# Optimization experiments

Hardware: AMD Instinct MI355X
Metric: run time of the kernel (lower is better)

The kernel has to match this reference:

```python
import jax, jax.numpy as jnp
import numpy as np

N = 50000      # nodes
E = 800000     # edges
IN = 128       # in_channels
HID = 128      # hidden_channels
R = 8          # num_relations
B = 4          # num_bases
EPS = 1e-5     # BatchNorm eps


def setup_inputs() -> dict:
    key = jax.random.key(0)
    ks = jax.random.split(key, 16)
    s = 0.05
    f = jnp.float32
    return {
        "x": jax.random.normal(ks[0], (N, IN), f),
        "edge_index": jax.random.randint(ks[1], (2, E), 0, N),
        "edge_type": jax.random.randint(ks[2], (E,), 0, R),
        # conv1 (RGCNConv with basis decomposition): W_r = sum_b comp[r,b] * bases[b]
        "comp1": jax.random.normal(ks[3], (R, B), f) * s,
        "bases1": jax.random.normal(ks[4], (B, IN, HID), f) * s,
        "root1": jax.random.normal(ks[5], (IN, HID), f) * s,
        "bias1": jnp.zeros((HID,), f),
        # skip1: Linear(in, hidden)
        "skip1_w": jax.random.normal(ks[6], (IN, HID), f) * s,
        "skip1_b": jnp.zeros((HID,), f),
        # BatchNorm(hidden)
        "bn_gamma": jnp.ones((HID,), f),
        "bn_beta": jnp.zeros((HID,), f),
        # conv2
        "comp2": jax.random.normal(ks[7], (R, B), f) * s,
        "bases2": jax.random.normal(ks[8], (B, HID, HID), f) * s,
        "root2": jax.random.normal(ks[9], (HID, HID), f) * s,
        "bias2": jnp.zeros((HID,), f),
        # skip2: Linear(hidden, hidden)
        "skip2_w": jax.random.normal(ks[10], (HID, HID), f) * s,
        "skip2_b": jnp.zeros((HID,), f),
    }


def rgcn_conv(x, src, dst, etype, comp, bases, root, bias):
    """PyG RGCNConv: per-relation mean aggregation + root weight + bias."""
    # Basis decomposition: W [R, d_in, d_out]
    W = jnp.einsum('rb,bdf->rdf', comp, bases)
    # Transform all nodes under every relation (node-level GEMM, avoids [E,B,F])
    h = jnp.einsum('nd,rdf->rnf', x, W)          # [R, N, F]
    msg = h[etype, src]                           # [E, F] gather per edge
    # mean per (dst, relation): normalize by relation-specific in-degree
    seg = dst * R + etype                         # combined segment id
    cnt = jax.ops.segment_sum(jnp.ones((msg.shape[0],), x.dtype), seg,
                              num_segments=N * R)
    msg = msg * (1.0 / jnp.maximum(cnt, 1.0))[seg][:, None]
    agg = jax.ops.segment_sum(msg, dst, num_segments=N)  # sum over relations
    return agg + x @ root + bias


def reference(x, edge_index, edge_type,
              comp1, bases1, root1, bias1, skip1_w, skip1_b,
              bn_gamma, bn_beta,
              comp2, bases2, root2, bias2, skip2_w, skip2_b):
    src, dst = edge_index[0], edge_index[1]
    # layer 1: conv + skip
    x1 = rgcn_conv(x, src, dst, edge_type, comp1, bases1, root1, bias1) \
         + x @ skip1_w + skip1_b
    h = x1  # captured pre-BatchNorm (i == num_layers - 1 branch)
    # BatchNorm (training-style batch stats) + ReLU; dropout = identity (eval)
    m = x1.mean(axis=0)
    v = x1.var(axis=0)
    xn = bn_gamma * (x1 - m) / jnp.sqrt(v + EPS) + bn_beta
    xr = jax.nn.relu(xn)
    # final layer: conv + skip
    x2 = rgcn_conv(xr, src, dst, edge_type, comp2, bases2, root2, bias2) \
         + xr @ skip2_w + skip2_b
    return (h, x2)
```

## Files before the change

kernel.cpp:

```cpp
#include <hip/hip_runtime.h>
#include <hip/hip_bf16.h>

#define Nn   50000
#define Ee   800000
#define RR   8
#define CAP  64
#define EPSV 1e-5f
#define NBLK 1563
#define NSLICE 8
#define SLICE_N 6250

typedef unsigned int   u32;
typedef unsigned short u16;
typedef __attribute__((ext_vector_type(8))) short bf16x8;
typedef __attribute__((ext_vector_type(4))) float f32x4;

typedef __attribute__((address_space(1))) const void gvoid;
typedef __attribute__((address_space(3))) void lvoid;

__device__ __forceinline__ void gl_lds16(const void* g, void* l) {
    __builtin_amdgcn_global_load_lds((gvoid*)g, (lvoid*)l, 16, 0, 0);
}

__device__ __forceinline__ float bf2f(u16 u) {
    return __uint_as_float(((u32)u) << 16);
}
__device__ __forceinline__ u16 f2bf(float f) {
    u32 x = __float_as_uint(f);
    u32 r = (x + 0x7FFFu + ((x >> 16) & 1u)) >> 16;
    return (u16)r;
}
__device__ __forceinline__ u32 pack2(float a, float b) {
    return (u32)f2bf(a) | ((u32)f2bf(b) << 16);
}

__global__ void __launch_bounds__(256) setup(
        const float2* __restrict__ xf, u32* __restrict__ xb,
        const int* __restrict__ ei, const int* __restrict__ et,
        int* __restrict__ deg, int* __restrict__ buckets,
        const float* __restrict__ bases1, const float* __restrict__ root1,
        const float* __restrict__ skip1w, u16* __restrict__ wt1,
        const float* __restrict__ bases2, const float* __restrict__ root2,
        const float* __restrict__ skip2w, u16* __restrict__ wt2) {
    int b = blockIdx.x;
    if (b < 12500) {
        int t = b * 256 + threadIdx.x;
        float2 v = xf[t];
        xb[t] = pack2(v.x, v.y);
    } else if (b < 37500) {
        int bb = b - 12500;
        int slice = bb & 7;
        int e = (bb >> 3) * 256 + threadIdx.x;
        int dst = ei[Ee + e];
        if ((u32)(dst - slice * SLICE_N) < (u32)SLICE_N) {
            int src = ei[e];
            int rt  = et[e];
            int idx = atomicAdd(&deg[dst], 1);
            if (idx < CAP)
                buckets[dst * CAP + idx] = (src & 0xFFFF) | (rt << 16);
        }
    } else {
        const float *bs, *ro, *sk; u16* wt; int t;
        if (b < 37820) { t = (b - 37500) * 256 + threadIdx.x; bs = bases1; ro = root1; sk = skip1w; wt = wt1; }
        else           { t = (b - 37820) * 256 + threadIdx.x; bs = bases2; ro = root2; sk = skip2w; wt = wt2; }
        int c = t / 640, k = t % 640;
        float v;
        if (k < 512) {
            int bb = k >> 7, kk = k & 127;
            v = bs[(bb * 128 + kk) * 128 + c];
        } else {
            int kk = k - 512;
            v = ro[kk * 128 + c] + sk[kk * 128 + c];
        }
        wt[c * 640 + k] = f2bf(v);
    }
}

__global__ void __launch_bounds__(256, 8) aggregate(const u32* __restrict__ xrow,
                                                    const float* __restrict__ comp,
                                                    const int* __restrict__ deg,
                                                    const int* __restrict__ buckets,
                                                    u32* __restrict__ xcat) {
    __shared__ int   bk_s[4][CAP];
    __shared__ float scale_s[4][32];
    int wv = threadIdx.x >> 6, lane = threadIdx.x & 63;
    int node = blockIdx.x * 4 + wv;

    int d = deg[node];
    d = d < CAP ? d : CAP;
    const int* bk = buckets + node * CAP;

    int w0 = 0;
    if (lane < d) { w0 = bk[lane]; bk_s[wv][lane] = w0; }

    int rt0 = (lane < d) ? (w0 >> 16) : 8;
    int c[RR];
#pragma unroll
    for (int r = 0; r < RR; r++) c[r] = __popcll(__ballot(rt0 == r));

    if (lane < 32) {
        int cc = c[lane >> 2];
        scale_s[wv][lane] = comp[lane] / (float)(cc < 1 ? 1 : cc);
    }
    __syncthreads();

    float a0 = 0, a1 = 0, b0 = 0, b1 = 0, c0 = 0, c1 = 0, d0 = 0, d1 = 0;
    int i = 0;
    for (; i + 4 <= d; i += 4) {
        int e0 = bk_s[wv][i], e1 = bk_s[wv][i + 1];
        int e2 = bk_s[wv][i + 2], e3 = bk_s[wv][i + 3];
        u32 x0 = xrow[(e0 & 0xFFFF) * 64 + lane];
        u32 x1 = xrow[(e1 & 0xFFFF) * 64 + lane];
        u32 x2 = xrow[(e2 & 0xFFFF) * 64 + lane];
        u32 x3 = xrow[(e3 & 0xFFFF) * 64 + lane];
        f32x4 s0 = *(const f32x4*)&scale_s[wv][(e0 >> 16) * 4];
        f32x4 s1 = *(const f32x4*)&scale_s[wv][(e1 >> 16) * 4];
        f32x4 s2 = *(const f32x4*)&scale_s[wv][(e2 >> 16) * 4];
        f32x4 s3 = *(const f32x4*)&scale_s[wv][(e3 >> 16) * 4];
        float v0, v1;
        v0 = bf2f((u16)x0); v1 = bf2f((u16)(x0 >> 16));
        a0 += s0[0] * v0; a1 += s0[0] * v1; b0 += s0[1] * v0; b1 += s0[1] * v1;
        c0 += s0[2] * v0; c1 += s0[2] * v1; d0 += s0[3] * v0; d1 += s0[3] * v1;
        v0 = bf2f((u16)x1); v1 = bf2f((u16)(x1 >> 16));
        a0 += s1[0] * v0; a1 += s1[0] * v1; b0 += s1[1] * v0; b1 += s1[1] * v1;
        c0 += s1[2] * v0; c1 += s1[2] * v1; d0 += s1[3] * v0; d1 += s1[3] * v1;
        v0 = bf2f((u16)x2); v1 = bf2f((u16)(x2 >> 16));
        a0 += s2[0] * v0; a1 += s2[0] * v1; b0 += s2[1] * v0; b1 += s2[1] * v1;
        c0 += s2[2] * v0; c1 += s2[2] * v1; d0 += s2[3] * v0; d1 += s2[3] * v1;
        v0 = bf2f((u16)x3); v1 = bf2f((u16)(x3 >> 16));
        a0 += s3[0] * v0; a1 += s3[0] * v1; b0 += s3[1] * v0; b1 += s3[1] * v1;
        c0 += s3[2] * v0; c1 += s3[2] * v1; d0 += s3[3] * v0; d1 += s3[3] * v1;
    }
    for (; i < d; i++) {
        int ee = bk_s[wv][i];
        u32 xv = xrow[(ee & 0xFFFF) * 64 + lane];
        f32x4 ss = *(const f32x4*)&scale_s[wv][(ee >> 16) * 4];
        float v0 = bf2f((u16)xv), v1 = bf2f((u16)(xv >> 16));
        a0 += ss[0] * v0; a1 += ss[0] * v1; b0 += ss[1] * v0; b1 += ss[1] * v1;
        c0 += ss[2] * v0; c1 += ss[2] * v1; d0 += ss[3] * v0; d1 += ss[3] * v1;
    }

    u32* orow = xcat + node * 256;
    orow[0 * 64 + lane] = pack2(a0, a1);
    orow[1 * 64 + lane] = pack2(b0, b1);
    orow[2 * 64 + lane] = pack2(c0, c1);
    orow[3 * 64 + lane] = pack2(d0, d1);
}

__global__ void __launch_bounds__(256) gemm_x(const u16* __restrict__ xcat,
                                              const u16* __restrict__ xrow,
                                              const u16* __restrict__ wt,
                                              const float* __restrict__ biasA,
                                              const float* __restrict__ biasB,
                                              float* __restrict__ out,
                                              float* __restrict__ bnsum,
                                              int do_stats) {
    __shared__ u16 As[32 * 64];
    __shared__ u16 Bs[128 * 64];

    int t = threadIdx.x, w = t >> 6, lane = t & 63;
    int m0 = blockIdx.x * 32;
    int lm = lane & 15, hk = lane >> 4;

    const u16* agp; const u16* axp; char* alp;
    {
        int f = t;
        int row = f >> 3, kc = (f & 7) ^ (row & 7);
        int gr = m0 + row; gr = gr < Nn ? gr : Nn - 1;
        agp = xcat + gr * 512 + kc * 8;
        axp = xrow + gr * 128 + kc * 8;
        alp = (char*)As + w * 1024;
    }
    const u16* bgp[4]; char* blp[4];
#pragma unroll
    for (int j = 0; j < 4; j++) {
        int f = j * 256 + t;
        int col = f >> 3, kc = (f & 7) ^ (col & 7);
        bgp[j] = wt + col * 640 + kc * 8;
        blp[j] = (char*)Bs + j * 4096 + w * 1024;
    }

    int wr = (w & 1) * 16, wc = (w >> 1) * 64;
    f32x4 acc[4];
#pragma unroll
    for (int g = 0; g < 4; g++) acc[g] = (f32x4){0, 0, 0, 0};

    for (int it = 0; it < 10; it++) {
        if (it < 8) gl_lds16(agp + it * 64, alp);
        else        gl_lds16(axp + (it - 8) * 64, alp);
        int kb = it * 64;
#pragma unroll
        for (int j = 0; j < 4; j++) gl_lds16(bgp[j] + kb, blp[j]);
        __syncthreads();
#pragma unroll
        for (int ks = 0; ks < 2; ks++) {
            int sw = (((ks * 4 + hk) ^ (lm & 7)) * 16);
            bf16x8 a0 = *(const bf16x8*)((const char*)As + (wr + lm) * 128 + sw);
            bf16x8 b0 = *(const bf16x8*)((const char*)Bs + (wc + lm) * 128 + sw);
            bf16x8 b1 = *(const bf16x8*)((const char*)Bs + (wc + 16 + lm) * 128 + sw);
            bf16x8 b2 = *(const bf16x8*)((const char*)Bs + (wc + 32 + lm) * 128 + sw);
            bf16x8 b3 = *(const bf16x8*)((const char*)Bs + (wc + 48 + lm) * 128 + sw);
            acc[0] = __builtin_amdgcn_mfma_f32_16x16x32_bf16(a0, b0, acc[0], 0, 0, 0);
            acc[1] = __builtin_amdgcn_mfma_f32_16x16x32_bf16(a0, b1, acc[1], 0, 0, 0);
            acc[2] = __builtin_amdgcn_mfma_f32_16x16x32_bf16(a0, b2, acc[2], 0, 0, 0);
            acc[3] = __builtin_amdgcn_mfma_f32_16x16x32_bf16(a0, b3, acc[3], 0, 0, 0);
        }
        __syncthreads();
    }

    float bias[4];
#pragma unroll
    for (int g = 0; g < 4; g++) {
        int cc = wc + g * 16 + lm;
        bias[g] = biasA[cc] + biasB[cc];
    }
    float lsum[4] = {0, 0, 0, 0}, lsq[4] = {0, 0, 0, 0};
#pragma unroll
    for (int g = 0; g < 4; g++)
#pragma unroll
        for (int i = 0; i < 4; i++) {
            int grow = m0 + wr + hk * 4 + i;
            if (grow < Nn) {
                float v = acc[g][i] + bias[g];
                out[grow * 128 + wc + g * 16 + lm] = v;
                lsum[g] += v; lsq[g] += v * v;
            }
        }
    if (do_stats) {
#pragma unroll
        for (int g = 0; g < 4; g++) {
            lsum[g] += __shfl_xor(lsum[g], 16); lsum[g] += __shfl_xor(lsum[g], 32);
            lsq[g]  += __shfl_xor(lsq[g], 16);  lsq[g]  += __shfl_xor(lsq[g], 32);
        }
        if (hk == 0) {
#pragma unroll
            for (int g = 0; g < 4; g++) {
                int cc = wc + g * 16 + lm;
                atomicAdd(&bnsum[cc], lsum[g]);
                atomicAdd(&bnsum[128 + cc], lsq[g]);
            }
        }
    }
}

__global__ void __launch_bounds__(256) bn_relu(const float2* __restrict__ h,
                                               const float* __restrict__ bnsum,
                                               const float* __restrict__ gamma,
                                               const float* __restrict__ beta,
                                               u32* __restrict__ xr) {
    __shared__ float ab_s[256];
    int tid = threadIdx.x;
    if (tid < 128) {
        float m   = bnsum[tid] * (1.0f / Nn);
        float ex2 = bnsum[128 + tid] * (1.0f / Nn);
        float var = ex2 - m * m;
        float s   = gamma[tid] * rsqrtf(var + EPSV);
        ab_s[tid]       = s;
        ab_s[128 + tid] = beta[tid] - m * s;
    }
    __syncthreads();
    int t = blockIdx.x * 256 + tid;
    int c0 = (tid & 63) * 2;
    float2 hv = h[t];
    float v0 = hv.x * ab_s[c0] + ab_s[128 + c0];
    float v1 = hv.y * ab_s[c0 + 1] + ab_s[128 + c0 + 1];
    v0 = v0 > 0.f ? v0 : 0.f;
    v1 = v1 > 0.f ? v1 : 0.f;
    xr[t] = pack2(v0, v1);
}

extern "C" void kernel_launch(void* const* d_in, const int* in_sizes, int n_in,
                              void* d_out, int out_size, void* d_ws, size_t ws_size,
                              hipStream_t stream) {
    const float* x      = (const float*)d_in[0];
    const int*   ei     = (const int*)d_in[1];
    const int*   et     = (const int*)d_in[2];
    const float* comp1  = (const float*)d_in[3];
    const float* bases1 = (const float*)d_in[4];
    const float* root1  = (const float*)d_in[5];
    const float* bias1  = (const float*)d_in[6];
    const float* skip1w = (const float*)d_in[7];
    const float* skip1b = (const float*)d_in[8];
    const float* gamma  = (const float*)d_in[9];
    const float* beta   = (const float*)d_in[10];
    const float* comp2  = (const float*)d_in[11];
    const float* bases2 = (const float*)d_in[12];
    const float* root2  = (const float*)d_in[13];
    const float* bias2  = (const float*)d_in[14];
    const float* skip2w = (const float*)d_in[15];
    const float* skip2b = (const float*)d_in[16];
    float* out = (float*)d_out;

    char* ws = (char*)d_ws;
    int*   deg     = (int*)(ws + 0);
    float* bnsum   = (float*)(ws + 200000);
    int*   buckets = (int*)(ws + 202240);
    u16*   wt1     = (u16*)(ws + 13002240);
    u16*   wt2     = (u16*)(ws + 13166080);
    u32*   xb      = (u32*)(ws + 13329920);
    u32*   xr      = xb;
    u16*   xcat    = (u16*)(ws + 26129920);

    hipMemsetAsync(deg, 0, 201024, stream);

    setup<<<38140, 256, 0, stream>>>((const float2*)x, xb, ei, et, deg, buckets,
                                     bases1, root1, skip1w, wt1,
                                     bases2, root2, skip2w, wt2);

    aggregate<<<Nn / 4, 256, 0, stream>>>(xb, comp1, deg, buckets, (u32*)xcat);
    gemm_x<<<NBLK, 256, 0, stream>>>(xcat, (const u16*)xb, wt1, bias1, skip1b,
                                     out, bnsum, 1);

    bn_relu<<<Nn / 4, 256, 0, stream>>>((const float2*)out, bnsum, gamma, beta, xr);

    aggregate<<<Nn / 4, 256, 0, stream>>>(xr, comp2, deg, buckets, (u32*)xcat);
    gemm_x<<<NBLK, 256, 0, stream>>>(xcat, (const u16*)xr, wt2, bias2, skip2b,
                                     out + Nn * 128, bnsum, 0);
}
```

Baseline: 344.8 us.

## Rewrite gemm_x as LDS-free per-wave 32x128 tiles with direct global loads

New measurement: 364.0 us. 5.6% more time.

```diff
diff --git a/kernel.cpp b/kernel.cpp
--- a/kernel.cpp
+++ b/kernel.cpp
@@ -6,7 +6,7 @@
 #define RR   8
 #define CAP  64
 #define EPSV 1e-5f
-#define NBLK 1563
+#define NBLK 391
 #define NSLICE 8
 #define SLICE_N 6250
 
@@ -17,10 +17,6 @@
 
 typedef __attribute__((address_space(1))) const void gvoid;
 typedef __attribute__((address_space(3))) void lvoid;
-
-__device__ __forceinline__ void gl_lds16(const void* g, void* l) {
-    __builtin_amdgcn_global_load_lds((gvoid*)g, (lvoid*)l, 16, 0, 0);
-}
 
 __device__ __forceinline__ float bf2f(u16 u) {
     return __uint_as_float(((u32)u) << 16);
@@ -147,95 +143,84 @@
     orow[3 * 64 + lane] = pack2(d0, d1);
 }
 
-__global__ void __launch_bounds__(256) gemm_x(const u16* __restrict__ xcat,
-                                              const u16* __restrict__ xrow,
-                                              const u16* __restrict__ wt,
-                                              const float* __restrict__ biasA,
-                                              const float* __restrict__ biasB,
-                                              float* __restrict__ out,
-                                              float* __restrict__ bnsum,
-                                              int do_stats) {
-    __shared__ u16 As[32 * 64];
-    __shared__ u16 Bs[128 * 64];
-
+__global__ void __launch_bounds__(256, 1) gemm_x(const u16* __restrict__ xcat,
+                                                 const u16* __restrict__ xrow,
+                                                 const u16* __restrict__ wt,
+                                                 const float* __restrict__ biasA,
+                                                 const float* __restrict__ biasB,
+                                                 float* __restrict__ out,
+                                                 float* __restrict__ bnsum,
+                                                 int do_stats) {
     int t = threadIdx.x, w = t >> 6, lane = t & 63;
-    int m0 = blockIdx.x * 32;
     int lm = lane & 15, hk = lane >> 4;
-
-    const u16* agp; const u16* axp; char* alp;
-    {
-        int f = t;
-        int row = f >> 3, kc = (f & 7) ^ (row & 7);
-        int gr = m0 + row; gr = gr < Nn ? gr : Nn - 1;
-        agp = xcat + gr * 512 + kc * 8;
-        axp = xrow + gr * 128 + kc * 8;
-        alp = (char*)As + w * 1024;
-    }
-    const u16* bgp[4]; char* blp[4];
-#pragma unroll
-    for (int j = 0; j < 4; j++) {
-        int f = j * 256 + t;
-        int col = f >> 3, kc = (f & 7) ^ (col & 7);
-        bgp[j] = wt + col * 640 + kc * 8;
-        blp[j] = (char*)Bs + j * 4096 + w * 1024;
-    }
-
-    int wr = (w & 1) * 16, wc = (w >> 1) * 64;
-    f32x4 acc[4];
-#pragma unroll
-    for (int g = 0; g < 4; g++) acc[g] = (f32x4){0, 0, 0, 0};
-
+    int mw = (blockIdx.x * 4 + w) * 32;
+
+    int r0 = mw + lm;      r0 = r0 < Nn ? r0 : Nn - 1;
+    int r1 = mw + 16 + lm; r1 = r1 < Nn ? r1 : Nn - 1;
+    const u16* a0p = xcat + r0 * 512 + hk * 8;
+    const u16* a1p = xcat + r1 * 512 + hk * 8;
+    const u16* x0p = xrow + r0 * 128 + hk * 8;
+    const u16* x1p = xrow + r1 * 128 + hk * 8;
+    const u16* bp  = wt + lm * 640 + hk * 8;
+
+    f32x4 acc[2][8];
+#pragma unroll
+    for (int fr = 0; fr < 2; fr++)
+#pragma unroll
+        for (int g = 0; g < 8; g++) acc[fr][g] = (f32x4){0, 0, 0, 0};
+
+#pragma unroll
     for (int it = 0; it < 10; it++) {
-        if (it < 8) gl_lds16(agp + it * 64, alp);
-        else        gl_lds16(axp + (it - 8) * 64, alp);
-        int kb = it * 64;
-#pragma unroll
-        for (int j = 0; j < 4; j++) gl_lds16(bgp[j] + kb, blp[j]);
-        __syncthreads();
 #pragma unroll
         for (int ks = 0; ks < 2; ks++) {
-            int sw = (((ks * 4 + hk) ^ (lm & 7)) * 16);
-            bf16x8 a0 = *(const bf16x8*)((const char*)As + (wr + lm) * 128 + sw);
-            bf16x8 b0 = *(const bf16x8*)((const char*)Bs + (wc + lm) * 128 + sw);
-            bf16x8 b1 = *(const bf16x8*)((const char*)Bs + (wc + 16 + lm) * 128 + sw);
-            bf16x8 b2 = *(const bf16x8*)((const char*)Bs + (wc + 32 + lm) * 128 + sw);
-            bf16x8 b3 = *(const bf16x8*)((const char*)Bs + (wc + 48 + lm) * 128 + sw);
-            acc[0] = __builtin_amdgcn_mfma_f32_16x16x32_bf16(a0, b0, acc[0], 0, 0, 0);
-            acc[1] = __builtin_amdgcn_mfma_f32_16x16x32_bf16(a0, b1, acc[1], 0, 0, 0);
-            acc[2] = __builtin_amdgcn_mfma_f32_16x16x32_bf16(a0, b2, acc[2], 0, 0, 0);
-            acc[3] = __builtin_amdgcn_mfma_f32_16x16x32_bf16(a0, b3, acc[3], 0, 0, 0);
-        }
-        __syncthreads();
-    }
-
-    float bias[4];
-#pragma unroll
-    for (int g = 0; g < 4; g++) {
-        int cc = wc + g * 16 + lm;
-        bias[g] = biasA[cc] + biasB[cc];
-    }
-    float lsum[4] = {0, 0, 0, 0}, lsq[4] = {0, 0, 0, 0};
-#pragma unroll
-    for (int g = 0; g < 4; g++)
-#pragma unroll
-        for (int i = 0; i < 4; i++) {
-            int grow = m0 + wr + hk * 4 + i;
-            if (grow < Nn) {
-                float v = acc[g][i] + bias[g];
-                out[grow * 128 + wc + g * 16 + lm] = v;
-                lsum[g] += v; lsq[g] += v * v;
+            int ko = it * 64 + ks * 32;
+            bf16x8 a0, a1;
+            if (it < 8) {
+                a0 = *(const bf16x8*)(a0p + ko);
+                a1 = *(const bf16x8*)(a1p + ko);
+            } else {
+                int kx = (it - 8) * 64 + ks * 32;
+                a0 = *(const bf16x8*)(x0p + kx);
+                a1 = *(const bf16x8*)(x1p + kx);
             }
+#pragma unroll
+            for (int g = 0; g < 8; g++) {
+                bf16x8 b = *(const bf16x8*)(bp + g * 10240 + ko);
+                acc[0][g] = __builtin_amdgcn_mfma_f32_16x16x32_bf16(a0, b, acc[0][g], 0, 0, 0);
+                acc[1][g] = __builtin_amdgcn_mfma_f32_16x16x32_bf16(a1, b, acc[1][g], 0, 0, 0);
+            }
+        }
+    }
+
+    float lsum[8], lsq[8];
+#pragma unroll
+    for (int g = 0; g < 8; g++) { lsum[g] = 0.f; lsq[g] = 0.f; }
+#pragma unroll
+    for (int fr = 0; fr < 2; fr++)
+#pragma unroll
+        for (int g = 0; g < 8; g++) {
+            int cc = g * 16 + lm;
+            float bias = biasA[cc] + biasB[cc];
+#pragma unroll
+            for (int i = 0; i < 4; i++) {
+                int grow = mw + fr * 16 + hk * 4 + i;
+                if (grow < Nn) {
+                    float v = acc[fr][g][i] + bias;
+                    out[grow * 128 + cc] = v;
+                    lsum[g] += v; lsq[g] += v * v;
+                }
+            }
         }
     if (do_stats) {
 #pragma unroll
-        for (int g = 0; g < 4; g++) {
+        for (int g = 0; g < 8; g++) {
             lsum[g] += __shfl_xor(lsum[g], 16); lsum[g] += __shfl_xor(lsum[g], 32);
             lsq[g]  += __shfl_xor(lsq[g], 16);  lsq[g]  += __shfl_xor(lsq[g], 32);
         }
         if (hk == 0) {
 #pragma unroll
-            for (int g = 0; g < 4; g++) {
-                int cc = wc + g * 16 + lm;
+            for (int g = 0; g < 8; g++) {
+                int cc = g * 16 + lm;
                 atomicAdd(&bnsum[cc], lsum[g]);
                 atomicAdd(&bnsum[128 + cc], lsq[g]);
             }
```
